# Kernel tuning notes

Measured on AMD Instinct MI355X. Metric: run time of the kernel, lower is better.

The kernel has to match this reference:

```python
import jax, jax.numpy as jnp
import numpy as np

INPUT_CHANNELS = 6
RESERVOIR_SIZE = 256
SPECTRAL_RADIUS = 0.9
SPARSITY = 0.8
BATCH = 256
SEQ_LEN = 512


def _make_reservoir_weights(seed=0):
    rng = np.random.RandomState(seed)
    W_res = rng.randn(RESERVOIR_SIZE, RESERVOIR_SIZE).astype(np.float32)
    mask = (rng.rand(RESERVOIR_SIZE, RESERVOIR_SIZE) > SPARSITY).astype(np.float32)
    W_res = W_res * mask
    cur_radius = np.abs(np.linalg.eigvals(W_res)).max()
    if cur_radius > 0:
        W_res = W_res * (SPECTRAL_RADIUS / cur_radius)
    return W_res.astype(np.float32)


def setup_inputs() -> dict:
    key = jax.random.key(0)
    k_x, k_in = jax.random.split(key)
    x = jax.random.normal(k_x, (BATCH, SEQ_LEN, INPUT_CHANNELS), dtype=jnp.float32)
    W_in = jax.random.normal(k_in, (INPUT_CHANNELS, RESERVOIR_SIZE), dtype=jnp.float32) * 0.1
    W_res = jnp.asarray(_make_reservoir_weights())
    return {"x": x, "W_in": W_in, "W_res": W_res}


def reference(x, W_in, W_res):
    # x: [B, T, C] -> x_proj: [B, T, R]
    x_proj = jnp.einsum("btc,cr->btr", x, W_in)
    B = x.shape[0]
    R = W_res.shape[0]
    h0 = jnp.zeros((B, R), dtype=x.dtype)

    def step(h, xp_t):
        # xp_t: [B, R]
        h_new = jnp.tanh(xp_t + h @ W_res)
        return h_new, h_new

    # scan over time: xs must be time-major [T, B, R]
    _, h_seq = jax.lax.scan(step, h0, jnp.swapaxes(x_proj, 0, 1))
    return jnp.swapaxes(h_seq, 0, 1)  # [B, T, R]
```

## Files before the change

kernel.cpp:

```cpp
#include <hip/hip_runtime.h>

#define BATCH 256
#define SEQ_T 512
#define CIN   6
#define RES   256
#define NCH     8
#define CSTRIDE 36
#define HBUF    (NCH * CSTRIDE)

typedef float f32x2 __attribute__((ext_vector_type(2)));

__device__ __forceinline__ f32x2 pk_fma(f32x2 a, f32x2 b, f32x2 c) {
    f32x2 d;
    asm("v_pk_fma_f32 %0, %1, %2, %3" : "=v"(d) : "v"(a), "v"(b), "v"(c));
    return d;
}

template <int CTRL>
__device__ __forceinline__ float dpp_add(float v) {
    union { float f; int i; } u;
    u.f = v;
    u.i = __builtin_amdgcn_mov_dpp(u.i, CTRL, 0xF, 0xF, true);
    return v + u.f;
}

__global__ __launch_bounds__(1024, 1)
void esn_scan_kernel(const float* __restrict__ x,
                     const float* __restrict__ W_in,
                     const float* __restrict__ W_res,
                     float* __restrict__ out) {
    __shared__ float h[2][HBUF];

    const int tid  = threadIdx.x;
    const int b    = blockIdx.x;
    const int lane = tid & 63;
    const int wid  = tid >> 6;
    const int sub  = lane & 7;
    const int rg   = lane >> 3;

    const int rbase = (wid << 4) | (rg << 1);

    f32x2 w2[2][16];
    #pragma unroll
    for (int a = 0; a < 2; ++a)
        #pragma unroll
        for (int j = 0; j < 16; ++j) {
            f32x2 p;
            p.x = W_res[(sub * 32 + 2 * j)     * RES + rbase + a];
            p.y = W_res[(sub * 32 + 2 * j + 1) * RES + rbase + a];
            w2[a][j] = p;
        }

    const int ract = rbase + (sub & 1);
    float win[CIN];
    #pragma unroll
    for (int c = 0; c < CIN; ++c) win[c] = W_in[c * RES + ract];

    if (tid < HBUF) h[0][tid] = 0.0f;
    __syncthreads();

    const float* xb = x + (size_t)b * SEQ_T * CIN;
    float*       ob = out + (size_t)b * SEQ_T * RES + ract;

    const float4* hr0 = (const float4*)&h[0][sub * CSTRIDE];
    const float4* hr1 = (const float4*)&h[1][sub * CSTRIDE];
    const int wslot = ((ract >> 5) * CSTRIDE) + (ract & 31);
    float* hw0 = &h[0][wslot];
    float* hw1 = &h[1][wslot];
    const bool writer = (sub < 2);

    float xA[CIN], xB[CIN];
    #pragma unroll
    for (int c = 0; c < CIN; ++c) xA[c] = xb[c];
    xb += CIN;

#define ESN_STEP(HRD, HWR, XC, XN, PREF)                                \
    {                                                                   \
        float4 hv[NCH];                                                 \
        _Pragma("unroll")                                               \
        for (int j = 0; j < NCH; ++j) hv[j] = (HRD)[j];                 \
        if (PREF) {                                                     \
            _Pragma("unroll")                                           \
            for (int c = 0; c < CIN; ++c) (XN)[c] = xb[c];              \
            xb += CIN;                                                  \
        }                                                               \
        f32x2 acc0 = {0.f, 0.f}, acc1 = {0.f, 0.f};                    \
        _Pragma("unroll")                                               \
        for (int j = 0; j < NCH; ++j) {                                 \
            f32x2 plo, phi;                                             \
            plo.x = hv[j].x; plo.y = hv[j].y;                           \
            phi.x = hv[j].z; phi.y = hv[j].w;                           \
            acc0 = pk_fma(plo, w2[0][2 * j],     acc0);                 \
            acc0 = pk_fma(phi, w2[0][2 * j + 1], acc0);                 \
            acc1 = pk_fma(plo, w2[1][2 * j],     acc1);                 \
            acc1 = pk_fma(phi, w2[1][2 * j + 1], acc1);                 \
        }                                                               \
        float a0 = acc0.x + acc0.y;                                     \
        float a1 = acc1.x + acc1.y;                                     \
        a0 = dpp_add<0xB1>(a0);  a1 = dpp_add<0xB1>(a1);                \
        a0 = dpp_add<0x4E>(a0);  a1 = dpp_add<0x4E>(a1);                \
        a0 = dpp_add<0x141>(a0); a1 = dpp_add<0x141>(a1);               \
        float s = (sub & 1) ? a1 : a0;                                  \
        if (writer) {                                                   \
            _Pragma("unroll")                                           \
            for (int c = 0; c < CIN; ++c) s = fmaf((XC)[c], win[c], s); \
            float e  = __expf(2.0f * s);                                \
            float hn = 1.0f - 2.0f * __builtin_amdgcn_rcpf(e + 1.0f);   \
            *(HWR) = hn;                                                \
            *ob = hn;                                                   \
        }                                                               \
        ob += RES;                                                      \
        asm volatile("s_waitcnt lgkmcnt(0)" ::: "memory");              \
        __builtin_amdgcn_s_barrier();                                   \
        asm volatile("" ::: "memory");                                  \
    }

    for (int t = 0; t < SEQ_T - 2; t += 2) {
        ESN_STEP(hr0, hw1, xA, xB, 1);
        ESN_STEP(hr1, hw0, xB, xA, 1);
    }
    ESN_STEP(hr0, hw1, xA, xB, 1);
    ESN_STEP(hr1, hw0, xB, xA, 0);
#undef ESN_STEP
}

extern "C" void kernel_launch(void* const* d_in, const int* in_sizes, int n_in,
                              void* d_out, int out_size, void* d_ws, size_t ws_size,
                              hipStream_t stream) {
    const float* x     = (const float*)d_in[0];
    const float* W_in  = (const float*)d_in[1];
    const float* W_res = (const float*)d_in[2];
    float*       out   = (float*)d_out;

    esn_scan_kernel<<<BATCH, 1024, 0, stream>>>(x, W_in, W_res, out);
}
```

Baseline: 466.2 us.

## Halve block size with 16-way K split and transpose-style DPP reduction

Each block now uses 512 threads instead of 1024. Each 16-lane group computes 8 output neurons over a 16-element slice of h, with the partial sums combined by a butterfly exchange-add DPP reduction. Two blocks may share a CU, and each barrier now syncs fewer waves, which is meant to cut per-step barrier and reduction overhead. In exchange each lane does more FMAs and keeps more weights in registers (64 f32x2), and the shared h layout changes to 16 chunks of stride 20.

```diff
diff --git a/kernel.cpp b/kernel.cpp
--- a/kernel.cpp
+++ b/kernel.cpp
@@ -4,8 +4,8 @@
 #define SEQ_T 512
 #define CIN   6
 #define RES   256
-#define NCH     8
-#define CSTRIDE 36
+#define NCH     16
+#define CSTRIDE 20
 #define HBUF    (NCH * CSTRIDE)
 
 typedef float f32x2 __attribute__((ext_vector_type(2)));
@@ -24,7 +24,15 @@
     return v + u.f;
 }
 
-__global__ __launch_bounds__(1024, 1)
+template <int CTRL>
+__device__ __forceinline__ float dpp_xadd(float keep, float give) {
+    union { float f; int i; } u;
+    u.f = give;
+    u.i = __builtin_amdgcn_mov_dpp(u.i, CTRL, 0xF, 0xF, true);
+    return keep + u.f;
+}
+
+__global__ __launch_bounds__(512, 2)
 void esn_scan_kernel(const float* __restrict__ x,
                      const float* __restrict__ W_in,
                      const float* __restrict__ W_res,
@@ -35,23 +43,24 @@
     const int b    = blockIdx.x;
     const int lane = tid & 63;
     const int wid  = tid >> 6;
-    const int sub  = lane & 7;
-    const int rg   = lane >> 3;
+    const int sub  = lane & 15;
+    const int g    = lane >> 4;
+    const int a    = lane & 7;
 
-    const int rbase = (wid << 4) | (rg << 1);
+    const int rbase = 32 * wid + 8 * g;
+    const int ract  = rbase + a;
 
-    f32x2 w2[2][16];
+    f32x2 w2[8][8];
     #pragma unroll
-    for (int a = 0; a < 2; ++a)
+    for (int o = 0; o < 8; ++o)
         #pragma unroll
-        for (int j = 0; j < 16; ++j) {
+        for (int m = 0; m < 8; ++m) {
             f32x2 p;
-            p.x = W_res[(sub * 32 + 2 * j)     * RES + rbase + a];
-            p.y = W_res[(sub * 32 + 2 * j + 1) * RES + rbase + a];
-            w2[a][j] = p;
+            p.x = W_res[(sub * 16 + 2 * m)     * RES + rbase + o];
+            p.y = W_res[(sub * 16 + 2 * m + 1) * RES + rbase + o];
+            w2[o][m] = p;
         }
 
-    const int ract = rbase + (sub & 1);
     float win[CIN];
     #pragma unroll
     for (int c = 0; c < CIN; ++c) win[c] = W_in[c * RES + ract];
@@ -64,10 +73,13 @@
 
     const float4* hr0 = (const float4*)&h[0][sub * CSTRIDE];
     const float4* hr1 = (const float4*)&h[1][sub * CSTRIDE];
-    const int wslot = ((ract >> 5) * CSTRIDE) + (ract & 31);
+    const int wslot = ((ract >> 4) * CSTRIDE) + (ract & 15);
     float* hw0 = &h[0][wslot];
     float* hw1 = &h[1][wslot];
-    const bool writer = (sub < 2);
+    const bool writer = (sub < 8);
+    const bool p0 = (lane & 1) != 0;
+    const bool p1 = (lane & 2) != 0;
+    const bool p2 = (lane & 4) != 0;
 
     float xA[CIN], xB[CIN];
     #pragma unroll
@@ -76,31 +88,41 @@
 
 #define ESN_STEP(HRD, HWR, XC, XN, PREF)                                \
     {                                                                   \
-        float4 hv[NCH];                                                 \
-        _Pragma("unroll")                                               \
-        for (int j = 0; j < NCH; ++j) hv[j] = (HRD)[j];                 \
+        float4 hv0 = (HRD)[0], hv1 = (HRD)[1], hv2 = (HRD)[2], hv3 = (HRD)[3]; \
         if (PREF) {                                                     \
             _Pragma("unroll")                                           \
             for (int c = 0; c < CIN; ++c) (XN)[c] = xb[c];              \
             xb += CIN;                                                  \
         }                                                               \
-        f32x2 acc0 = {0.f, 0.f}, acc1 = {0.f, 0.f};                    \
-        _Pragma("unroll")                                               \
-        for (int j = 0; j < NCH; ++j) {                                 \
-            f32x2 plo, phi;                                             \
-            plo.x = hv[j].x; plo.y = hv[j].y;                           \
-            phi.x = hv[j].z; phi.y = hv[j].w;                           \
-            acc0 = pk_fma(plo, w2[0][2 * j],     acc0);                 \
-            acc0 = pk_fma(phi, w2[0][2 * j + 1], acc0);                 \
-            acc1 = pk_fma(plo, w2[1][2 * j],     acc1);                 \
-            acc1 = pk_fma(phi, w2[1][2 * j + 1], acc1);                 \
+        f32x2 hp[8];                                                    \
+        hp[0].x = hv0.x; hp[0].y = hv0.y; hp[1].x = hv0.z; hp[1].y = hv0.w; \
+        hp[2].x = hv1.x; hp[2].y = hv1.y; hp[3].x = hv1.z; hp[3].y = hv1.w; \
+        hp[4].x = hv2.x; hp[4].y = hv2.y; hp[5].x = hv2.z; hp[5].y = hv2.w; \
+        hp[6].x = hv3.x; hp[6].y = hv3.y; hp[7].x = hv3.z; hp[7].y = hv3.w; \
+        float s0, s1, s2, s3, s4, s5, s6, s7;                           \
+        {                                                               \
+            f32x2 acc[8];                                               \
+            _Pragma("unroll")                                           \
+            for (int o = 0; o < 8; ++o) {                               \
+                f32x2 t = {0.f, 0.f};                                   \
+                _Pragma("unroll")                                       \
+                for (int m = 0; m < 8; ++m) t = pk_fma(hp[m], w2[o][m], t); \
+                acc[o] = t;                                             \
+            }                                                           \
+            s0 = acc[0].x + acc[0].y; s1 = acc[1].x + acc[1].y;         \
+            s2 = acc[2].x + acc[2].y; s3 = acc[3].x + acc[3].y;         \
+            s4 = acc[4].x + acc[4].y; s5 = acc[5].x + acc[5].y;         \
+            s6 = acc[6].x + acc[6].y; s7 = acc[7].x + acc[7].y;         \
         }                                                               \
-        float a0 = acc0.x + acc0.y;                                     \
-        float a1 = acc1.x + acc1.y;                                     \
-        a0 = dpp_add<0xB1>(a0);  a1 = dpp_add<0xB1>(a1);                \
-        a0 = dpp_add<0x4E>(a0);  a1 = dpp_add<0x4E>(a1);                \
-        a0 = dpp_add<0x141>(a0); a1 = dpp_add<0x141>(a1);               \
-        float s = (sub & 1) ? a1 : a0;                                  \
+          \
+        float t0 = dpp_xadd<0xB1>(p0 ? s1 : s0, p0 ? s0 : s1);          \
+        float t1 = dpp_xadd<0xB1>(p0 ? s3 : s2, p0 ? s2 : s3);          \
+        float t2 = dpp_xadd<0xB1>(p0 ? s5 : s4, p0 ? s4 : s5);          \
+        float t3 = dpp_xadd<0xB1>(p0 ? s7 : s6, p0 ? s6 : s7);          \
+        float u0 = dpp_xadd<0x4E>(p1 ? t1 : t0, p1 ? t0 : t1);          \
+        float u1 = dpp_xadd<0x4E>(p1 ? t3 : t2, p1 ? t2 : t3);          \
+        float v  = dpp_xadd<0x124>(p2 ? u1 : u0, p2 ? u0 : u1);         \
+        float s  = dpp_add<0x128>(v);                                   \
         if (writer) {                                                   \
             _Pragma("unroll")                                           \
             for (int c = 0; c < CIN; ++c) s = fmaf((XC)[c], win[c], s); \
@@ -132,5 +154,5 @@
     const float* W_res = (const float*)d_in[2];
     float*       out   = (float*)d_out;
 
-    esn_scan_kernel<<<BATCH, 1024, 0, stream>>>(x, W_in, W_res, out);
+    esn_scan_kernel<<<BATCH, 512, 0, stream>>>(x, W_in, W_res, out);
 }
```

Result: faster. 431.1 us (-7.5%).
